# Performance work log

Hardware: AMD Instinct MI355X
Metric: run time of the kernel (lower is better)

## Reference

```python
import jax, jax.numpy as jnp
import numpy as np

L, N, C = 128, 32, 128
DIM_MLP, OUT = 128, 128


def setup_inputs() -> dict:
    key = jax.random.key(0)
    ks = jax.random.split(key, 6)
    s_in2 = 1.0 / np.sqrt(2 * C)
    s_mid = 1.0 / np.sqrt(DIM_MLP)
    s_in = 1.0 / np.sqrt(C)
    return {
        "x": jax.random.normal(ks[0], (L, N, C), jnp.float32),
        "attn_w1": jax.random.normal(ks[1], (2 * C, DIM_MLP), jnp.float32) * s_in2,
        "attn_b1": jnp.zeros((DIM_MLP,), jnp.float32),
        "attn_w2": jax.random.normal(ks[2], (DIM_MLP, OUT), jnp.float32) * s_mid,
        "attn_b2": jnp.zeros((OUT,), jnp.float32),
        "value_w1": jax.random.normal(ks[3], (C, DIM_MLP), jnp.float32) * s_in,
        "value_b1": jnp.zeros((DIM_MLP,), jnp.float32),
        "value_w2": jax.random.normal(ks[4], (DIM_MLP, OUT), jnp.float32) * s_mid,
        "value_b2": jnp.zeros((OUT,), jnp.float32),
    }


def reference(x, attn_w1, attn_b1, attn_w2, attn_b2,
              value_w1, value_b1, value_w2, value_b2):
    l, n, c = x.shape
    # Outer concat: pair[i, j, b] = concat(x[i, b], x[j, b])  -> (l, l, N, 2C)
    xi = jnp.broadcast_to(x[:, None, :, :], (l, l, n, c))
    xj = jnp.broadcast_to(x[None, :, :, :], (l, l, n, c))
    pair = jnp.concatenate([xi, xj], axis=-1)
    # Pairwise attention MLP (ReLU hidden, linear output)
    h = jax.nn.relu(pair @ attn_w1 + attn_b1)          # (l, l, N, dim_mlp)
    attn = h @ attn_w2 + attn_b2                       # (l, l, N, out)
    # Value MLP
    hv = jax.nn.relu(x @ value_w1 + value_b1)          # (l, N, dim_mlp)
    value = hv @ value_w2 + value_b2                   # (l, N, out)
    # Elementwise weighted reduce over key axis j (NOT a matmul over channels)
    out = jnp.einsum('ijbc,jbc->ibc', attn, value)     # (l, N, out)
    return out
```

## Files before the change

### kernel.cpp

```cpp
#include <hip/hip_runtime.h>
#include <hip/hip_bf16.h>

#define L_DIM 128
#define N_DIM 32
#define C_DIM 128
#define K_DIM 128
#define OUT_DIM 128

typedef __attribute__((ext_vector_type(8))) short short8;
typedef __attribute__((ext_vector_type(4))) float float4v;

static __device__ __forceinline__ short bf16_bits(float f) {
    __bf16 h = (__bf16)f;
    return __builtin_bit_cast(short, h);
}

static __device__ __forceinline__ void gl_lds16(const float* g, float* l) {
    __builtin_amdgcn_global_load_lds(
        (const __attribute__((address_space(1))) unsigned int*)g,
        (__attribute__((address_space(3))) unsigned int*)l, 16, 0, 0);
}

__global__ __launch_bounds__(256) void k_pre(
    const float* __restrict__ x,
    const float* __restrict__ attn_w1, const float* __restrict__ attn_b1,
    const float* __restrict__ attn_w2,
    const float* __restrict__ value_w1, const float* __restrict__ value_b1,
    const float* __restrict__ value_w2, const float* __restrict__ value_b2,
    float* __restrict__ P, float* __restrict__ Q, float* __restrict__ Vt,
    short* __restrict__ W2s)
{
    int bid = blockIdx.x;
    if (bid >= 512) {
        int e = (bid - 512) * 256 + threadIdx.x;
        int idx  = e & 7;
        int colr = (e >> 3) & 15;
        int quad = (e >> 7) & 3;
        int mi   = (e >> 9) & 3;
        int ct   = e >> 11;
        int k = quad * 8 + 32 * mi + idx;
        int c = ct * 16 + colr;
        W2s[e] = bf16_bits(attn_w2[k * OUT_DIM + c]);
        return;
    }

    __shared__ float xs[8][C_DIM];
    __shared__ float hvs[8][K_DIM];
    int tid = threadIdx.x;
    int b   = bid >> 4;
    int i0g = (bid & 15) * 8;

    {
        int f = tid * 4;
        int row = f >> 7, c = f & 127;
        *(float4v*)(&xs[row][c]) =
            *(const float4v*)(x + ((size_t)(i0g + row) * N_DIM + b) * C_DIM + c);
    }
    __syncthreads();

    int ks   = tid & 127;
    int half = tid >> 7;

    float pacc[4] = {0,0,0,0};
    float qacc[4] = {0,0,0,0};
    float hacc[4] = {0,0,0,0};
    #pragma unroll 4
    for (int c = 0; c < C_DIM; ++c) {
        float wa = attn_w1[c * K_DIM + ks];
        float wb = attn_w1[(C_DIM + c) * K_DIM + ks];
        float wv = value_w1[c * K_DIM + ks];
        #pragma unroll
        for (int r = 0; r < 4; ++r) {
            float xr = xs[half * 4 + r][c];
            pacc[r] = fmaf(xr, wa, pacc[r]);
            qacc[r] = fmaf(xr, wb, qacc[r]);
            hacc[r] = fmaf(xr, wv, hacc[r]);
        }
    }
    float b1 = attn_b1[ks], vb1 = value_b1[ks];
    #pragma unroll
    for (int r = 0; r < 4; ++r) {
        int i = i0g + half * 4 + r;
        P[((size_t)b * L_DIM + i) * K_DIM + ks] = pacc[r];
        Q[((size_t)b * L_DIM + i) * K_DIM + ks] = qacc[r] + b1;
        hvs[half * 4 + r][ks] = fmaxf(hacc[r] + vb1, 0.f);
    }
    __syncthreads();

    float vacc[4] = {0,0,0,0};
    #pragma unroll 4
    for (int k = 0; k < K_DIM; ++k) {
        float w = value_w2[k * OUT_DIM + ks];
        #pragma unroll
        for (int r = 0; r < 4; ++r)
            vacc[r] = fmaf(hvs[half * 4 + r][k], w, vacc[r]);
    }
    float vb2 = value_b2[ks];
    float4v vout = { vacc[0] + vb2, vacc[1] + vb2, vacc[2] + vb2, vacc[3] + vb2 };
    *(float4v*)(Vt + ((size_t)b * OUT_DIM + ks) * L_DIM + i0g + half * 4) = vout;
}

__global__ __launch_bounds__(256)
__attribute__((amdgpu_waves_per_eu(2)))
void k_main(
    const float* __restrict__ P, const float* __restrict__ Q,
    const float* __restrict__ Vt,
    const short* __restrict__ W2s, const float* __restrict__ attn_b2,
    float* __restrict__ out)
{
    __shared__ float Q_lds[3][2048];
    __shared__ float V_lds[2][2048];
    __shared__ float P_lds[512];

    int b    = blockIdx.x >> 5;
    int it4  = blockIdx.x & 31;
    int tid  = threadIdx.x;
    int wave = tid >> 6;
    int lane = tid & 63;
    int quad = lane >> 4;
    int col  = lane & 15;
    int ip   = wave >> 1;
    int cth  = wave & 1;

    const float* Qbase = Q  + (size_t)b * L_DIM * K_DIM;
    const float* Vbase = Vt + (size_t)b * OUT_DIM * L_DIM;

    short8 bfrag[4][4];
    const short8* w2p = (const short8*)W2s;
    #pragma unroll
    for (int cl = 0; cl < 4; ++cl)
        #pragma unroll
        for (int mi = 0; mi < 4; ++mi)
            bfrag[cl][mi] =
                w2p[(((cth * 4 + cl) * 4 + mi) * 4 + quad) * 16 + col];

    int qsrc[2], vsrc[2];
    #pragma unroll
    for (int t = 0; t < 2; ++t) {
        int n = (t * 4 + wave) * 64 + lane;
        qsrc[t] = (n & 15) * K_DIM + (n >> 4) * 4;
        int c = n >> 2, s = n & 3;
        vsrc[t] = c * L_DIM + ((s ^ (c & 3)) << 2);
    }

    auto stageQ = [&](int jt, int buf) {
        #pragma unroll
        for (int t = 0; t < 2; ++t)
            gl_lds16(Qbase + jt * 16 * K_DIM + qsrc[t],
                     &Q_lds[buf][(t * 4 + wave) * 256]);
    };
    auto stageV = [&](int jt, int buf) {
        #pragma unroll
        for (int t = 0; t < 2; ++t)
            gl_lds16(Vbase + jt * 16 + vsrc[t],
                     &V_lds[buf][(t * 4 + wave) * 256]);
    };

    stageQ(0, 0);
    stageQ(1, 1);
    stageV(0, 0);
    if (wave == 0) {
        const float* Pbase = P + ((size_t)b * L_DIM + it4 * 4) * K_DIM;
        gl_lds16(Pbase + lane * 4,       &P_lds[0]);
        gl_lds16(Pbase + 256 + lane * 4, &P_lds[256]);
    }
    __syncthreads();

    float acc0[4] = {0.f, 0.f, 0.f, 0.f};
    float acc1[4] = {0.f, 0.f, 0.f, 0.f};
    float sv[4]   = {0.f, 0.f, 0.f, 0.f};
    int pofs = 0;

    short8 af[2][2][4];

    auto build = [&](int jt, int p) {
        const float* qb = &Q_lds[jt % 3][col * 4];
        const float* Pr = &P_lds[(ip * 2) * 128 + quad * 8 + pofs];
        #pragma unroll
        for (int ksl = 0; ksl < 4; ++ksl) {
            int kc0 = (ksl * 4 + quad) * 2;
            float4v q0 = *(const float4v*)(qb + kc0 * 64);
            float4v q1 = *(const float4v*)(qb + kc0 * 64 + 64);
            #pragma unroll
            for (int ii = 0; ii < 2; ++ii) {
                const float* Pc = Pr + ii * 128 + ksl * 32;
                float4v s0 = *(const float4v*)Pc + q0;
                float4v s1 = *(const float4v*)(Pc + 4) + q1;
                short8 a;
                #pragma unroll
                for (int t = 0; t < 4; ++t) {
                    a[t]     = bf16_bits(fmaxf(s0[t], 0.f));
                    a[t + 4] = bf16_bits(fmaxf(s1[t], 0.f));
                }
                af[p][ii][ksl] = a;
            }
        }
    };

    build(0, 0);

    #pragma unroll
    for (int r = 0; r < 8; ++r) {
        asm volatile("" : "+v"(pofs));
        if (r < 6) stageQ(r + 2, (r + 2) % 3);
        if (r < 7) stageV(r + 1, (r + 1) & 1);

        if (r < 7) build(r + 1, (r + 1) & 1);

        const float* Vc = &V_lds[r & 1][0];
        #pragma unroll
        for (int cl = 0; cl < 4; ++cl) {
            float4v c40 = {0.f, 0.f, 0.f, 0.f};
            float4v c41 = {0.f, 0.f, 0.f, 0.f};
            #pragma unroll
            for (int ksl = 0; ksl < 4; ++ksl) {
                c40 = __builtin_amdgcn_mfma_f32_16x16x32_bf16(
                        af[r & 1][0][ksl], bfrag[cl][ksl], c40, 0, 0, 0);
                c41 = __builtin_amdgcn_mfma_f32_16x16x32_bf16(
                        af[r & 1][1][ksl], bfrag[cl][ksl], c41, 0, 0, 0);
            }
            int cc = cth * 64 + cl * 16 + col;
            float4v vv = *(const float4v*)
                (Vc + cc * 16 + ((quad ^ (cc & 3)) << 2));
            #pragma unroll
            for (int rr = 0; rr < 4; ++rr) {
                acc0[cl] = fmaf(c40[rr], vv[rr], acc0[cl]);
                acc1[cl] = fmaf(c41[rr], vv[rr], acc1[cl]);
                sv[cl]  += vv[rr];
            }
        }

        if (r < 7) __syncthreads();
    }

    #pragma unroll
    for (int cl = 0; cl < 4; ++cl) {
        acc0[cl] += __shfl_xor(acc0[cl], 16, 64);
        acc0[cl] += __shfl_xor(acc0[cl], 32, 64);
        acc1[cl] += __shfl_xor(acc1[cl], 16, 64);
        acc1[cl] += __shfl_xor(acc1[cl], 32, 64);
        sv[cl]   += __shfl_xor(sv[cl], 16, 64);
        sv[cl]   += __shfl_xor(sv[cl], 32, 64);
    }

    if (quad == 0) {
        int i0 = it4 * 4 + ip * 2;
        #pragma unroll
        for (int cl = 0; cl < 4; ++cl) {
            int cc = cth * 64 + cl * 16 + col;
            float bsv = attn_b2[cc] * sv[cl];
            out[((size_t)i0 * N_DIM + b) * OUT_DIM + cc]       = acc0[cl] + bsv;
            out[((size_t)(i0 + 1) * N_DIM + b) * OUT_DIM + cc] = acc1[cl] + bsv;
        }
    }
}

extern "C" void kernel_launch(void* const* d_in, const int* in_sizes, int n_in,
                              void* d_out, int out_size, void* d_ws, size_t ws_size,
                              hipStream_t stream)
{
    const float* x        = (const float*)d_in[0];
    const float* attn_w1  = (const float*)d_in[1];
    const float* attn_b1  = (const float*)d_in[2];
    const float* attn_w2  = (const float*)d_in[3];
    const float* attn_b2  = (const float*)d_in[4];
    const float* value_w1 = (const float*)d_in[5];
    const float* value_b1 = (const float*)d_in[6];
    const float* value_w2 = (const float*)d_in[7];
    const float* value_b2 = (const float*)d_in[8];
    float* out = (float*)d_out;

    float* ws  = (float*)d_ws;
    float* P   = ws;
    float* Q   = ws + 524288;
    float* Vt  = ws + 1048576;
    short* W2s = (short*)(ws + 1572864);

    k_pre<<<576, 256, 0, stream>>>(x, attn_w1, attn_b1, attn_w2,
                                   value_w1, value_b1, value_w2, value_b2,
                                   P, Q, Vt, W2s);
    k_main<<<1024, 256, 0, stream>>>(P, Q, Vt, W2s, attn_b2, out);
}
```

Before: 124.4 us.

## Load Q and V directly into registers, drop LDS staging and barriers

The main kernel stops staging Q and V tiles through LDS with async global-to-LDS copies and per-iteration barriers. Each lane now loads its Q fragments (double-buffered in registers) and V values straight from global memory, relying on L2/L1 caching. This removes LDS traffic and the block-wide syncs, at the cost of more registers and uncoalesced, redundant global loads across waves. The pre-kernel also processes 16 rows per block instead of 8, halving its block count and reusing each weight load across more rows.

```diff
diff --git a/kernel.cpp b/kernel.cpp
--- a/kernel.cpp
+++ b/kernel.cpp
@@ -31,8 +31,8 @@
     short* __restrict__ W2s)
 {
     int bid = blockIdx.x;
-    if (bid >= 512) {
-        int e = (bid - 512) * 256 + threadIdx.x;
+    if (bid >= 256) {
+        int e = (bid - 256) * 256 + threadIdx.x;
         int idx  = e & 7;
         int colr = (e >> 3) & 15;
         int quad = (e >> 7) & 3;
@@ -44,34 +44,35 @@
         return;
     }
 
-    __shared__ float xs[8][C_DIM];
-    __shared__ float hvs[8][K_DIM];
+    __shared__ float xs[16][C_DIM];
+    __shared__ float hvs[16][K_DIM];
     int tid = threadIdx.x;
-    int b   = bid >> 4;
-    int i0g = (bid & 15) * 8;
+    int b   = bid >> 3;
+    int i0g = (bid & 7) * 16;
 
     {
-        int f = tid * 4;
+        int f = tid * 8;
         int row = f >> 7, c = f & 127;
-        *(float4v*)(&xs[row][c]) =
-            *(const float4v*)(x + ((size_t)(i0g + row) * N_DIM + b) * C_DIM + c);
+        const float* xp = x + ((size_t)(i0g + row) * N_DIM + b) * C_DIM + c;
+        *(float4v*)(&xs[row][c])     = *(const float4v*)xp;
+        *(float4v*)(&xs[row][c + 4]) = *(const float4v*)(xp + 4);
     }
     __syncthreads();
 
     int ks   = tid & 127;
     int half = tid >> 7;
 
-    float pacc[4] = {0,0,0,0};
-    float qacc[4] = {0,0,0,0};
-    float hacc[4] = {0,0,0,0};
+    float pacc[8] = {0,0,0,0,0,0,0,0};
+    float qacc[8] = {0,0,0,0,0,0,0,0};
+    float hacc[8] = {0,0,0,0,0,0,0,0};
     #pragma unroll 4
     for (int c = 0; c < C_DIM; ++c) {
         float wa = attn_w1[c * K_DIM + ks];
         float wb = attn_w1[(C_DIM + c) * K_DIM + ks];
         float wv = value_w1[c * K_DIM + ks];
         #pragma unroll
-        for (int r = 0; r < 4; ++r) {
-            float xr = xs[half * 4 + r][c];
+        for (int r = 0; r < 8; ++r) {
+            float xr = xs[half * 8 + r][c];
             pacc[r] = fmaf(xr, wa, pacc[r]);
             qacc[r] = fmaf(xr, wb, qacc[r]);
             hacc[r] = fmaf(xr, wv, hacc[r]);
@@ -79,25 +80,28 @@
     }
     float b1 = attn_b1[ks], vb1 = value_b1[ks];
     #pragma unroll
-    for (int r = 0; r < 4; ++r) {
-        int i = i0g + half * 4 + r;
+    for (int r = 0; r < 8; ++r) {
+        int i = i0g + half * 8 + r;
         P[((size_t)b * L_DIM + i) * K_DIM + ks] = pacc[r];
         Q[((size_t)b * L_DIM + i) * K_DIM + ks] = qacc[r] + b1;
-        hvs[half * 4 + r][ks] = fmaxf(hacc[r] + vb1, 0.f);
+        hvs[half * 8 + r][ks] = fmaxf(hacc[r] + vb1, 0.f);
     }
     __syncthreads();
 
-    float vacc[4] = {0,0,0,0};
+    float vacc[8] = {0,0,0,0,0,0,0,0};
     #pragma unroll 4
     for (int k = 0; k < K_DIM; ++k) {
         float w = value_w2[k * OUT_DIM + ks];
         #pragma unroll
-        for (int r = 0; r < 4; ++r)
-            vacc[r] = fmaf(hvs[half * 4 + r][k], w, vacc[r]);
+        for (int r = 0; r < 8; ++r)
+            vacc[r] = fmaf(hvs[half * 8 + r][k], w, vacc[r]);
     }
     float vb2 = value_b2[ks];
-    float4v vout = { vacc[0] + vb2, vacc[1] + vb2, vacc[2] + vb2, vacc[3] + vb2 };
-    *(float4v*)(Vt + ((size_t)b * OUT_DIM + ks) * L_DIM + i0g + half * 4) = vout;
+    float* vp = Vt + ((size_t)b * OUT_DIM + ks) * L_DIM + i0g + half * 8;
+    float4v v0 = { vacc[0] + vb2, vacc[1] + vb2, vacc[2] + vb2, vacc[3] + vb2 };
+    float4v v1 = { vacc[4] + vb2, vacc[5] + vb2, vacc[6] + vb2, vacc[7] + vb2 };
+    *(float4v*)vp       = v0;
+    *(float4v*)(vp + 4) = v1;
 }
 
 __global__ __launch_bounds__(256)
@@ -108,8 +112,6 @@
     const short* __restrict__ W2s, const float* __restrict__ attn_b2,
     float* __restrict__ out)
 {
-    __shared__ float Q_lds[3][2048];
-    __shared__ float V_lds[2][2048];
     __shared__ float P_lds[512];
 
     int b    = blockIdx.x >> 5;
@@ -122,9 +124,6 @@
     int ip   = wave >> 1;
     int cth  = wave & 1;
 
-    const float* Qbase = Q  + (size_t)b * L_DIM * K_DIM;
-    const float* Vbase = Vt + (size_t)b * OUT_DIM * L_DIM;
-
     short8 bfrag[4][4];
     const short8* w2p = (const short8*)W2s;
     #pragma unroll
@@ -134,31 +133,6 @@
             bfrag[cl][mi] =
                 w2p[(((cth * 4 + cl) * 4 + mi) * 4 + quad) * 16 + col];
 
-    int qsrc[2], vsrc[2];
-    #pragma unroll
-    for (int t = 0; t < 2; ++t) {
-        int n = (t * 4 + wave) * 64 + lane;
-        qsrc[t] = (n & 15) * K_DIM + (n >> 4) * 4;
-        int c = n >> 2, s = n & 3;
-        vsrc[t] = c * L_DIM + ((s ^ (c & 3)) << 2);
-    }
-
-    auto stageQ = [&](int jt, int buf) {
-        #pragma unroll
-        for (int t = 0; t < 2; ++t)
-            gl_lds16(Qbase + jt * 16 * K_DIM + qsrc[t],
-                     &Q_lds[buf][(t * 4 + wave) * 256]);
-    };
-    auto stageV = [&](int jt, int buf) {
-        #pragma unroll
-        for (int t = 0; t < 2; ++t)
-            gl_lds16(Vbase + jt * 16 + vsrc[t],
-                     &V_lds[buf][(t * 4 + wave) * 256]);
-    };
-
-    stageQ(0, 0);
-    stageQ(1, 1);
-    stageV(0, 0);
     if (wave == 0) {
         const float* Pbase = P + ((size_t)b * L_DIM + it4 * 4) * K_DIM;
         gl_lds16(Pbase + lane * 4,       &P_lds[0]);
@@ -166,21 +140,46 @@
     }
     __syncthreads();
 
+    const float* qa = Q  + (size_t)b * L_DIM * K_DIM + col * K_DIM + quad * 8;
+    const float* va = Vt + (size_t)b * OUT_DIM * L_DIM
+                         + (cth * 64 + col) * L_DIM + quad * 4;
+
     float acc0[4] = {0.f, 0.f, 0.f, 0.f};
     float acc1[4] = {0.f, 0.f, 0.f, 0.f};
     float sv[4]   = {0.f, 0.f, 0.f, 0.f};
     int pofs = 0;
 
-    short8 af[2][2][4];
-
-    auto build = [&](int jt, int p) {
-        const float* qb = &Q_lds[jt % 3][col * 4];
+    float4v qreg[2][4][2];
+    #pragma unroll
+    for (int ksl = 0; ksl < 4; ++ksl) {
+        qreg[0][ksl][0] = *(const float4v*)(qa + ksl * 32);
+        qreg[0][ksl][1] = *(const float4v*)(qa + ksl * 32 + 4);
+    }
+
+    #pragma unroll
+    for (int r = 0; r < 8; ++r) {
+        asm volatile("" : "+v"(pofs));
+
+        float4v vv[4];
+        #pragma unroll
+        for (int cl = 0; cl < 4; ++cl)
+            vv[cl] = *(const float4v*)(va + (size_t)cl * 16 * L_DIM + r * 16);
+
+        if (r < 7) {
+            const float* qn = qa + (r + 1) * 16 * K_DIM;
+            #pragma unroll
+            for (int ksl = 0; ksl < 4; ++ksl) {
+                qreg[(r + 1) & 1][ksl][0] = *(const float4v*)(qn + ksl * 32);
+                qreg[(r + 1) & 1][ksl][1] = *(const float4v*)(qn + ksl * 32 + 4);
+            }
+        }
+
+        short8 af[2][4];
         const float* Pr = &P_lds[(ip * 2) * 128 + quad * 8 + pofs];
         #pragma unroll
         for (int ksl = 0; ksl < 4; ++ksl) {
-            int kc0 = (ksl * 4 + quad) * 2;
-            float4v q0 = *(const float4v*)(qb + kc0 * 64);
-            float4v q1 = *(const float4v*)(qb + kc0 * 64 + 64);
+            float4v q0 = qreg[r & 1][ksl][0];
+            float4v q1 = qreg[r & 1][ksl][1];
             #pragma unroll
             for (int ii = 0; ii < 2; ++ii) {
                 const float* Pc = Pr + ii * 128 + ksl * 32;
@@ -192,22 +191,10 @@
                     a[t]     = bf16_bits(fmaxf(s0[t], 0.f));
                     a[t + 4] = bf16_bits(fmaxf(s1[t], 0.f));
                 }
-                af[p][ii][ksl] = a;
-            }
-        }
-    };
-
-    build(0, 0);
-
-    #pragma unroll
-    for (int r = 0; r < 8; ++r) {
-        asm volatile("" : "+v"(pofs));
-        if (r < 6) stageQ(r + 2, (r + 2) % 3);
-        if (r < 7) stageV(r + 1, (r + 1) & 1);
-
-        if (r < 7) build(r + 1, (r + 1) & 1);
-
-        const float* Vc = &V_lds[r & 1][0];
+                af[ii][ksl] = a;
+            }
+        }
+
         #pragma unroll
         for (int cl = 0; cl < 4; ++cl) {
             float4v c40 = {0.f, 0.f, 0.f, 0.f};
@@ -215,22 +202,17 @@
             #pragma unroll
             for (int ksl = 0; ksl < 4; ++ksl) {
                 c40 = __builtin_amdgcn_mfma_f32_16x16x32_bf16(
-                        af[r & 1][0][ksl], bfrag[cl][ksl], c40, 0, 0, 0);
+                        af[0][ksl], bfrag[cl][ksl], c40, 0, 0, 0);
                 c41 = __builtin_amdgcn_mfma_f32_16x16x32_bf16(
-                        af[r & 1][1][ksl], bfrag[cl][ksl], c41, 0, 0, 0);
-            }
-            int cc = cth * 64 + cl * 16 + col;
-            float4v vv = *(const float4v*)
-                (Vc + cc * 16 + ((quad ^ (cc & 3)) << 2));
+                        af[1][ksl], bfrag[cl][ksl], c41, 0, 0, 0);
+            }
             #pragma unroll
             for (int rr = 0; rr < 4; ++rr) {
-                acc0[cl] = fmaf(c40[rr], vv[rr], acc0[cl]);
-                acc1[cl] = fmaf(c41[rr], vv[rr], acc1[cl]);
-                sv[cl]  += vv[rr];
-            }
-        }
-
-        if (r < 7) __syncthreads();
+                acc0[cl] = fmaf(c40[rr], vv[cl][rr], acc0[cl]);
+                acc1[cl] = fmaf(c41[rr], vv[cl][rr], acc1[cl]);
+                sv[cl]  += vv[cl][rr];
+            }
+        }
     }
 
     #pragma unroll
@@ -276,7 +258,7 @@
     float* Vt  = ws + 1048576;
     short* W2s = (short*)(ws + 1572864);
 
-    k_pre<<<576, 256, 0, stream>>>(x, attn_w1, attn_b1, attn_w2,
+    k_pre<<<320, 256, 0, stream>>>(x, attn_w1, attn_b1, attn_w2,
                                    value_w1, value_b1, value_w2, value_b2,
                                    P, Q, Vt, W2s);
     k_main<<<1024, 256, 0, stream>>>(P, Q, Vt, W2s, attn_b2, out);
```

Result: slower. 144.8 us (+16.4%).
